# Kernel tuning notes

Hardware: AMD Instinct MI355X
Metric: run time of the kernel (lower is better)

The kernel has to match this reference:

```python
import jax, jax.numpy as jnp
import numpy as np

N_NODES = 100000
N_EDGES = 1600000
IN_DIM, HID_DIM, OUT_DIM = 512, 64, 32


def _gcn_conv(x, row, col, W, b, n):
    # GCNConv: h = x W; out[v] = sum_{(u,v)} norm(u,v) * h[u] + b
    # deg computed on destination (col) with self-loops already included.
    deg = jax.ops.segment_sum(jnp.ones_like(col, dtype=x.dtype), col, num_segments=n)
    dinv = jnp.where(deg > 0, jax.lax.rsqrt(deg), 0.0)
    norm = dinv[row] * dinv[col]                      # [E]
    h = x @ W                                          # [N, out]
    msg = h[row] * norm[:, None]                       # [E, out] gather
    out = jax.ops.segment_sum(msg, col, num_segments=n)  # scatter-add
    return out + b


def setup_inputs() -> dict:
    key = jax.random.key(0)
    k1, k2, k3, k4 = jax.random.split(key, 4)
    x = jax.random.normal(k1, (N_NODES, IN_DIM), dtype=jnp.float32)
    edge_index = jax.random.randint(k2, (2, N_EDGES), 0, N_NODES, dtype=jnp.int64)
    W1 = jax.random.normal(k3, (IN_DIM, HID_DIM), dtype=jnp.float32) / np.sqrt(IN_DIM)
    b1 = jnp.zeros((HID_DIM,), dtype=jnp.float32)
    W2 = jax.random.normal(k4, (HID_DIM, OUT_DIM), dtype=jnp.float32) / np.sqrt(HID_DIM)
    b2 = jnp.zeros((OUT_DIM,), dtype=jnp.float32)
    return {"x": x, "edge_index": edge_index, "W1": W1, "b1": b1, "W2": W2, "b2": b2}


def reference(x, edge_index, W1, b1, W2, b2):
    n = x.shape[0]
    # add self-loops (PyG GCNConv default add_self_loops=True)
    loop = jnp.arange(n, dtype=edge_index.dtype)
    row = jnp.concatenate([edge_index[0], loop])
    col = jnp.concatenate([edge_index[1], loop])
    h = _gcn_conv(x, row, col, W1, b1, n)
    h = jax.nn.relu(h)
    # dropout is identity in eval mode (training=False)
    h = _gcn_conv(h, row, col, W2, b2, n)
    return jax.nn.log_softmax(h, axis=1)
```

## Files before the change

### kernel.cpp

```cpp
#include <hip/hip_runtime.h>


#define IN_DIM 512
#define HID    64
#define OUTD   32

typedef __attribute__((ext_vector_type(8))) short bf16x8;
typedef __attribute__((ext_vector_type(4))) float floatx4;
typedef __attribute__((ext_vector_type(4))) unsigned short ushort4v;
typedef __attribute__((ext_vector_type(8))) unsigned short ushort8v;

__device__ __forceinline__ unsigned short f2bf(float f) {
    unsigned int u = __float_as_uint(f);
    unsigned int r = (u + 0x7fffu + ((u >> 16) & 1u)) >> 16;
    return (unsigned short)r;
}
__device__ __forceinline__ float bf2f(unsigned short h) {
    return __uint_as_float(((unsigned int)h) << 16);
}

__device__ __forceinline__ int eidx(const int* idx32, long long e, int is64) {
    if (is64) { const long long* p = (const long long*)idx32; return (int)p[e]; }
    return idx32[e];
}

__global__ void k_detect(const int* __restrict__ idx, int* __restrict__ flag) {
    if (blockIdx.x == 0 && threadIdx.x == 0) {
        int z = (idx[1] == 0) & (idx[3] == 0) & (idx[5] == 0) & (idx[7] == 0);
        *flag = z;
    }
}

__global__ void k_prepW(const float* __restrict__ W1,
                        unsigned short* __restrict__ W1t_hi,
                        unsigned short* __restrict__ W1t_lo) {
    int t = blockIdx.x * blockDim.x + threadIdx.x;
    if (t < 64 * 512) {
        int n = t >> 9, k = t & 511;
        float v = W1[k * HID + n];
        unsigned short h = f2bf(v);
        W1t_hi[t] = h;
        W1t_lo[t] = f2bf(v - bf2f(h));
    }
}

__global__ void k_zero(int* __restrict__ cnt, int N) {
    int i = blockIdx.x * blockDim.x + threadIdx.x;
    if (i < N) cnt[i] = 0;
}

__global__ void k_count(const int* __restrict__ idx, const int* __restrict__ flag,
                        int* __restrict__ cnt, int E) {
    int e = blockIdx.x * blockDim.x + threadIdx.x;
    if (e >= E) return;
    const int is64 = *flag;
    int c = eidx(idx, (long long)E + e, is64);
    atomicAdd(&cnt[c], 1);
}

__global__ void k_scanA(const int* __restrict__ cnt, int* __restrict__ rowptr,
                        int* __restrict__ part, int N) {
    __shared__ int s[256];
    const int t = threadIdx.x;
    const int i = blockIdx.x * 256 + t;
    int v = (i < N) ? cnt[i] : 0;
    s[t] = v;
    __syncthreads();
#pragma unroll
    for (int off = 1; off < 256; off <<= 1) {
        int x = (t >= off) ? s[t - off] : 0;
        __syncthreads();
        s[t] += x;
        __syncthreads();
    }
    if (i < N) rowptr[i] = s[t] - v;
    if (t == 255) part[blockIdx.x] = s[255];
}

__global__ void k_scanB(const int* __restrict__ part, int* __restrict__ partex, int nb) {
    __shared__ int s[1024];
    const int t = threadIdx.x;
    int v = (t < nb) ? part[t] : 0;
    s[t] = v;
    __syncthreads();
#pragma unroll
    for (int off = 1; off < 1024; off <<= 1) {
        int x = (t >= off) ? s[t - off] : 0;
        __syncthreads();
        s[t] += x;
        __syncthreads();
    }
    partex[t] = s[t] - v;
}

__global__ void k_scanC(int* __restrict__ rowptr, const int* __restrict__ partex,
                        int N, int E) {
    const int i = blockIdx.x * blockDim.x + threadIdx.x;
    if (i < N) rowptr[i] += partex[i >> 8];
    if (i == 0) rowptr[N] = E;
}

__global__ void k_dinv(const int* __restrict__ rowptr, float* __restrict__ dinv, int N) {
    int i = blockIdx.x * blockDim.x + threadIdx.x;
    if (i < N) dinv[i] = rsqrtf((float)(1 + rowptr[i + 1] - rowptr[i]));
}

__global__ void k_place(const int* __restrict__ idx, const int* __restrict__ flag,
                        int* __restrict__ cnt, const int* __restrict__ rowptr,
                        int* __restrict__ src, int E) {
    int e = blockIdx.x * blockDim.x + threadIdx.x;
    if (e >= E) return;
    const int is64 = *flag;
    int r = eidx(idx, e, is64);
    int c = eidx(idx, (long long)E + e, is64);
    int ofs = atomicAdd(&cnt[c], -1) - 1;
    src[rowptr[c] + ofs] = r;
}

__launch_bounds__(256)
__global__ void k_gemm1_mfma(const float* __restrict__ x,
                             const unsigned short* __restrict__ Wt_hi,
                             const unsigned short* __restrict__ Wt_lo,
                             const float* __restrict__ dinv,
                             float* __restrict__ g1, int N) {
    __shared__ unsigned short xs_hi[64 * 72];
    __shared__ unsigned short xs_lo[64 * 72];
    __shared__ unsigned short ws_hi[64 * 72];
    __shared__ unsigned short ws_lo[64 * 72];

    const int t = threadIdx.x;
    const int lane = t & 63;
    const int w = t >> 6;
    const int m = lane & 15;
    const int quad = lane >> 4;
    const int row_base = blockIdx.x * 64;

    const floatx4 zero = {0.0f, 0.0f, 0.0f, 0.0f};
    floatx4 acc[4] = {zero, zero, zero, zero};

    for (int kc = 0; kc < IN_DIM; kc += 64) {
        {
            const int kq = (t & 15) * 4;
#pragma unroll
            for (int p = 0; p < 4; ++p) {
                int rl = (t >> 4) + p * 16;
                int row = row_base + rl;
                if (row > N - 1) row = N - 1;
                float4 v = *(const float4*)(x + (size_t)row * IN_DIM + kc + kq);
                ushort4v hi, lo;
                hi.x = f2bf(v.x); lo.x = f2bf(v.x - bf2f(hi.x));
                hi.y = f2bf(v.y); lo.y = f2bf(v.y - bf2f(hi.y));
                hi.z = f2bf(v.z); lo.z = f2bf(v.z - bf2f(hi.z));
                hi.w = f2bf(v.w); lo.w = f2bf(v.w - bf2f(hi.w));
                *(ushort4v*)&xs_hi[rl * 72 + kq] = hi;
                *(ushort4v*)&xs_lo[rl * 72 + kq] = lo;
            }
        }
        {
            const int nl = t >> 2;
            const int q = (t & 3) * 16;
            const unsigned short* ph = Wt_hi + (size_t)nl * IN_DIM + kc + q;
            const unsigned short* pl = Wt_lo + (size_t)nl * IN_DIM + kc + q;
            *(ushort8v*)&ws_hi[nl * 72 + q]     = *(const ushort8v*)(ph);
            *(ushort8v*)&ws_hi[nl * 72 + q + 8] = *(const ushort8v*)(ph + 8);
            *(ushort8v*)&ws_lo[nl * 72 + q]     = *(const ushort8v*)(pl);
            *(ushort8v*)&ws_lo[nl * 72 + q + 8] = *(const ushort8v*)(pl + 8);
        }
        __syncthreads();
#pragma unroll
        for (int ks = 0; ks < 2; ++ks) {
            const int ko = ks * 32 + quad * 8;
            bf16x8 a_hi = *(const bf16x8*)&xs_hi[(w * 16 + m) * 72 + ko];
            bf16x8 a_lo = *(const bf16x8*)&xs_lo[(w * 16 + m) * 72 + ko];
#pragma unroll
            for (int nt = 0; nt < 4; ++nt) {
                bf16x8 b_hi = *(const bf16x8*)&ws_hi[(nt * 16 + m) * 72 + ko];
                bf16x8 b_lo = *(const bf16x8*)&ws_lo[(nt * 16 + m) * 72 + ko];
                acc[nt] = __builtin_amdgcn_mfma_f32_16x16x32_bf16(a_hi, b_hi, acc[nt], 0, 0, 0);
                acc[nt] = __builtin_amdgcn_mfma_f32_16x16x32_bf16(a_lo, b_hi, acc[nt], 0, 0, 0);
                acc[nt] = __builtin_amdgcn_mfma_f32_16x16x32_bf16(a_hi, b_lo, acc[nt], 0, 0, 0);
            }
        }
        __syncthreads();
    }
#pragma unroll
    for (int r = 0; r < 4; ++r) {
        const int row = row_base + w * 16 + quad * 4 + r;
        if (row < N) {
            const float dv = dinv[row];
#pragma unroll
            for (int nt = 0; nt < 4; ++nt)
                g1[(size_t)row * HID + nt * 16 + m] = acc[nt][r] * dv;
        }
    }
}

__launch_bounds__(256)
__global__ void k_agg1_gemm2(const int* __restrict__ rowptr, const int* __restrict__ src,
                             const float* __restrict__ g1, const float* __restrict__ W2,
                             const float* __restrict__ b1, const float* __restrict__ dinv,
                             float* __restrict__ g2, int N) {
    __shared__ float w2s[HID * OUTD];
    __shared__ float hs[4][HID];

    const int t = threadIdx.x;
    for (int i = t; i < HID * OUTD; i += 256) w2s[i] = W2[i];

    const int w = t >> 6, lane = t & 63;
    const int v = blockIdx.x * 4 + w;
    float dv = 0.0f;
    if (v < N) {
        float acc = g1[(size_t)v * HID + lane];
        int i = rowptr[v];
        const int end = rowptr[v + 1];
        for (; i + 1 < end; i += 2) {
            int r0 = src[i], r1 = src[i + 1];
            acc += g1[(size_t)r0 * HID + lane] + g1[(size_t)r1 * HID + lane];
        }
        if (i < end) acc += g1[(size_t)src[i] * HID + lane];
        dv = dinv[v];
        hs[w][lane] = fmaxf(fmaf(dv, acc, b1[lane]), 0.0f);
    }
    __syncthreads();
    if (v < N) {
        const int j = lane & 31, half = lane >> 5;
        float s = 0.0f;
#pragma unroll
        for (int k = 0; k < 32; ++k) {
            const int kk = half * 32 + k;
            s = fmaf(hs[w][kk], w2s[kk * OUTD + j], s);
        }
        s += __shfl_down(s, 32);
        if (lane < 32) g2[(size_t)v * OUTD + j] = s * dv;
    }
}

__global__ void k_out(const int* __restrict__ rowptr, const int* __restrict__ src,
                      const float* __restrict__ g2, const float* __restrict__ b2,
                      const float* __restrict__ dinv, float* __restrict__ out, int N) {
    const int v = blockIdx.x * 8 + (int)(threadIdx.x >> 5);
    const int j = threadIdx.x & 31;
    if (v >= N) return;
    float acc = g2[(size_t)v * OUTD + j];
    int i = rowptr[v];
    const int end = rowptr[v + 1];
    for (; i + 1 < end; i += 2) {
        int r0 = src[i], r1 = src[i + 1];
        acc += g2[(size_t)r0 * OUTD + j] + g2[(size_t)r1 * OUTD + j];
    }
    if (i < end) acc += g2[(size_t)src[i] * OUTD + j];
    const float z = fmaf(dinv[v], acc, b2[j]);
    float m = z;
#pragma unroll
    for (int d = 16; d; d >>= 1) m = fmaxf(m, __shfl_xor(m, d, 32));
    float s = expf(z - m);
#pragma unroll
    for (int d = 16; d; d >>= 1) s += __shfl_xor(s, d, 32);
    out[(size_t)v * OUTD + j] = z - m - logf(s);
}

extern "C" void kernel_launch(void* const* d_in, const int* in_sizes, int n_in,
                              void* d_out, int out_size, void* d_ws, size_t ws_size,
                              hipStream_t stream) {
    const float* x   = (const float*)d_in[0];
    const int*   idx = (const int*)d_in[1];
    const float* W1  = (const float*)d_in[2];
    const float* b1  = (const float*)d_in[3];
    const float* W2  = (const float*)d_in[4];
    const float* b2  = (const float*)d_in[5];
    float* out = (float*)d_out;

    const int N = in_sizes[0] / IN_DIM;
    const int E = in_sizes[1] / 2;

    unsigned short* W1t_hi = (unsigned short*)d_ws;
    unsigned short* W1t_lo = W1t_hi + 64 * 512;
    int* cnt    = (int*)(W1t_lo + 64 * 512);
    int* rowptr = cnt + N;
    int* part   = rowptr + (N + 4);
    int* partex = part + 1024;
    int* srcA   = partex + 1024;
    int* flag   = srcA + E;
    float* dinv = (float*)(flag + 4);
    float* g1   = dinv + N;
    float* g2   = g1 + (size_t)N * HID;

    const int B = 256;
    const int nb = (N + 255) / 256;

    k_detect<<<1, 64, 0, stream>>>(idx, flag);
    k_prepW<<<(64 * 512 + B - 1) / B, B, 0, stream>>>(W1, W1t_hi, W1t_lo);
    k_zero<<<(N + B - 1) / B, B, 0, stream>>>(cnt, N);
    k_count<<<(E + B - 1) / B, B, 0, stream>>>(idx, flag, cnt, E);
    k_scanA<<<nb, 256, 0, stream>>>(cnt, rowptr, part, N);
    k_scanB<<<1, 1024, 0, stream>>>(part, partex, nb);
    k_scanC<<<nb, 256, 0, stream>>>(rowptr, partex, N, E);
    k_dinv<<<(N + B - 1) / B, B, 0, stream>>>(rowptr, dinv, N);
    k_place<<<(E + B - 1) / B, B, 0, stream>>>(idx, flag, cnt, rowptr, srcA, E);

    k_gemm1_mfma<<<(N + 63) / 64, 256, 0, stream>>>(x, W1t_hi, W1t_lo, dinv, g1, N);
    k_agg1_gemm2<<<(N + 3) / 4, 256, 0, stream>>>(rowptr, srcA, g1, W2, b1, dinv, g2, N);
    k_out<<<(N + 7) / 8, B, 0, stream>>>(rowptr, srcA, g2, b2, dinv, out, N);
}
```

Before: 644.1 us.

## Store intermediates in fp16, merge setup kernels, single-workgroup scan, unroll gathers

Stores the intermediate feature tables g1 and g2 as fp16 instead of fp32, halving the bytes moved by the gather-heavy aggregation kernels. It also merges the flag-detect, W1-prep and zeroing kernels into one launch. The three-stage scan plus dinv kernel is replaced by a single 1024-thread workgroup scan that also writes dinv, and the gather loops are unrolled by four. Precision drops for the intermediates, and the serial per-thread scan chunks (about 98 elements each) may be slower than the parallel scan.

```diff
diff --git a/kernel.cpp b/kernel.cpp
--- a/kernel.cpp
+++ b/kernel.cpp
@@ -1,4 +1,5 @@
 #include <hip/hip_runtime.h>
+#include <hip/hip_fp16.h>
 
 
 #define IN_DIM 512
@@ -24,17 +25,17 @@
     return idx32[e];
 }
 
-__global__ void k_detect(const int* __restrict__ idx, int* __restrict__ flag) {
-    if (blockIdx.x == 0 && threadIdx.x == 0) {
+__global__ void k_init(const float* __restrict__ W1,
+                       unsigned short* __restrict__ W1t_hi,
+                       unsigned short* __restrict__ W1t_lo,
+                       const int* __restrict__ idx, int* __restrict__ flag,
+                       int* __restrict__ cnt, int N) {
+    int t = blockIdx.x * blockDim.x + threadIdx.x;
+    if (t == 0) {
         int z = (idx[1] == 0) & (idx[3] == 0) & (idx[5] == 0) & (idx[7] == 0);
         *flag = z;
     }
-}
-
-__global__ void k_prepW(const float* __restrict__ W1,
-                        unsigned short* __restrict__ W1t_hi,
-                        unsigned short* __restrict__ W1t_lo) {
-    int t = blockIdx.x * blockDim.x + threadIdx.x;
+    if (t < N) cnt[t] = 0;
     if (t < 64 * 512) {
         int n = t >> 9, k = t & 511;
         float v = W1[k * HID + n];
@@ -42,11 +43,6 @@
         W1t_hi[t] = h;
         W1t_lo[t] = f2bf(v - bf2f(h));
     }
-}
-
-__global__ void k_zero(int* __restrict__ cnt, int N) {
-    int i = blockIdx.x * blockDim.x + threadIdx.x;
-    if (i < N) cnt[i] = 0;
 }
 
 __global__ void k_count(const int* __restrict__ idx, const int* __restrict__ flag,
@@ -58,30 +54,16 @@
     atomicAdd(&cnt[c], 1);
 }
 
-__global__ void k_scanA(const int* __restrict__ cnt, int* __restrict__ rowptr,
-                        int* __restrict__ part, int N) {
-    __shared__ int s[256];
-    const int t = threadIdx.x;
-    const int i = blockIdx.x * 256 + t;
-    int v = (i < N) ? cnt[i] : 0;
-    s[t] = v;
-    __syncthreads();
-#pragma unroll
-    for (int off = 1; off < 256; off <<= 1) {
-        int x = (t >= off) ? s[t - off] : 0;
-        __syncthreads();
-        s[t] += x;
-        __syncthreads();
-    }
-    if (i < N) rowptr[i] = s[t] - v;
-    if (t == 255) part[blockIdx.x] = s[255];
-}
-
-__global__ void k_scanB(const int* __restrict__ part, int* __restrict__ partex, int nb) {
+__global__ void k_scan1wg(const int* __restrict__ cnt, int* __restrict__ rowptr,
+                          float* __restrict__ dinv, int N, int E) {
     __shared__ int s[1024];
     const int t = threadIdx.x;
-    int v = (t < nb) ? part[t] : 0;
-    s[t] = v;
+    const int chunk = (N + 1023) / 1024;
+    const int lo = t * chunk;
+    const int hi = (lo + chunk < N) ? lo + chunk : N;
+    int sum = 0;
+    for (int i = lo; i < hi; ++i) sum += cnt[i];
+    s[t] = sum;
     __syncthreads();
 #pragma unroll
     for (int off = 1; off < 1024; off <<= 1) {
@@ -90,19 +72,14 @@
         s[t] += x;
         __syncthreads();
     }
-    partex[t] = s[t] - v;
-}
-
-__global__ void k_scanC(int* __restrict__ rowptr, const int* __restrict__ partex,
-                        int N, int E) {
-    const int i = blockIdx.x * blockDim.x + threadIdx.x;
-    if (i < N) rowptr[i] += partex[i >> 8];
-    if (i == 0) rowptr[N] = E;
-}
-
-__global__ void k_dinv(const int* __restrict__ rowptr, float* __restrict__ dinv, int N) {
-    int i = blockIdx.x * blockDim.x + threadIdx.x;
-    if (i < N) dinv[i] = rsqrtf((float)(1 + rowptr[i + 1] - rowptr[i]));
+    int run = s[t] - sum;
+    for (int i = lo; i < hi; ++i) {
+        int c = cnt[i];
+        rowptr[i] = run;
+        dinv[i] = rsqrtf((float)(1 + c));
+        run += c;
+    }
+    if (t == 0) rowptr[N] = E;
 }
 
 __global__ void k_place(const int* __restrict__ idx, const int* __restrict__ flag,
@@ -122,7 +99,7 @@
                              const unsigned short* __restrict__ Wt_hi,
                              const unsigned short* __restrict__ Wt_lo,
                              const float* __restrict__ dinv,
-                             float* __restrict__ g1, int N) {
+                             __half* __restrict__ g1, int N) {
     __shared__ unsigned short xs_hi[64 * 72];
     __shared__ unsigned short xs_lo[64 * 72];
     __shared__ unsigned short ws_hi[64 * 72];
@@ -190,16 +167,16 @@
             const float dv = dinv[row];
 #pragma unroll
             for (int nt = 0; nt < 4; ++nt)
-                g1[(size_t)row * HID + nt * 16 + m] = acc[nt][r] * dv;
+                g1[(size_t)row * HID + nt * 16 + m] = __float2half(acc[nt][r] * dv);
         }
     }
 }
 
 __launch_bounds__(256)
 __global__ void k_agg1_gemm2(const int* __restrict__ rowptr, const int* __restrict__ src,
-                             const float* __restrict__ g1, const float* __restrict__ W2,
+                             const __half* __restrict__ g1, const float* __restrict__ W2,
                              const float* __restrict__ b1, const float* __restrict__ dinv,
-                             float* __restrict__ g2, int N) {
+                             __half* __restrict__ g2, int N) {
     __shared__ float w2s[HID * OUTD];
     __shared__ float hs[4][HID];
 
@@ -210,14 +187,18 @@
     const int v = blockIdx.x * 4 + w;
     float dv = 0.0f;
     if (v < N) {
-        float acc = g1[(size_t)v * HID + lane];
+        float acc = (float)g1[(size_t)v * HID + lane];
         int i = rowptr[v];
         const int end = rowptr[v + 1];
-        for (; i + 1 < end; i += 2) {
-            int r0 = src[i], r1 = src[i + 1];
-            acc += g1[(size_t)r0 * HID + lane] + g1[(size_t)r1 * HID + lane];
-        }
-        if (i < end) acc += g1[(size_t)src[i] * HID + lane];
+        for (; i + 3 < end; i += 4) {
+            int r0 = src[i], r1 = src[i + 1], r2 = src[i + 2], r3 = src[i + 3];
+            float a0 = (float)g1[(size_t)r0 * HID + lane];
+            float a1 = (float)g1[(size_t)r1 * HID + lane];
+            float a2 = (float)g1[(size_t)r2 * HID + lane];
+            float a3 = (float)g1[(size_t)r3 * HID + lane];
+            acc += (a0 + a1) + (a2 + a3);
+        }
+        for (; i < end; ++i) acc += (float)g1[(size_t)src[i] * HID + lane];
         dv = dinv[v];
         hs[w][lane] = fmaxf(fmaf(dv, acc, b1[lane]), 0.0f);
     }
@@ -231,24 +212,28 @@
             s = fmaf(hs[w][kk], w2s[kk * OUTD + j], s);
         }
         s += __shfl_down(s, 32);
-        if (lane < 32) g2[(size_t)v * OUTD + j] = s * dv;
+        if (lane < 32) g2[(size_t)v * OUTD + j] = __float2half(s * dv);
     }
 }
 
 __global__ void k_out(const int* __restrict__ rowptr, const int* __restrict__ src,
-                      const float* __restrict__ g2, const float* __restrict__ b2,
+                      const __half* __restrict__ g2, const float* __restrict__ b2,
                       const float* __restrict__ dinv, float* __restrict__ out, int N) {
     const int v = blockIdx.x * 8 + (int)(threadIdx.x >> 5);
     const int j = threadIdx.x & 31;
     if (v >= N) return;
-    float acc = g2[(size_t)v * OUTD + j];
+    float acc = (float)g2[(size_t)v * OUTD + j];
     int i = rowptr[v];
     const int end = rowptr[v + 1];
-    for (; i + 1 < end; i += 2) {
-        int r0 = src[i], r1 = src[i + 1];
-        acc += g2[(size_t)r0 * OUTD + j] + g2[(size_t)r1 * OUTD + j];
-    }
-    if (i < end) acc += g2[(size_t)src[i] * OUTD + j];
+    for (; i + 3 < end; i += 4) {
+        int r0 = src[i], r1 = src[i + 1], r2 = src[i + 2], r3 = src[i + 3];
+        float a0 = (float)g2[(size_t)r0 * OUTD + j];
+        float a1 = (float)g2[(size_t)r1 * OUTD + j];
+        float a2 = (float)g2[(size_t)r2 * OUTD + j];
+        float a3 = (float)g2[(size_t)r3 * OUTD + j];
+        acc += (a0 + a1) + (a2 + a3);
+    }
+    for (; i < end; ++i) acc += (float)g2[(size_t)src[i] * OUTD + j];
     const float z = fmaf(dinv[v], acc, b2[j]);
     float m = z;
 #pragma unroll
@@ -277,25 +262,17 @@
     unsigned short* W1t_lo = W1t_hi + 64 * 512;
     int* cnt    = (int*)(W1t_lo + 64 * 512);
     int* rowptr = cnt + N;
-    int* part   = rowptr + (N + 4);
-    int* partex = part + 1024;
-    int* srcA   = partex + 1024;
+    int* srcA   = rowptr + (N + 4);
     int* flag   = srcA + E;
     float* dinv = (float*)(flag + 4);
-    float* g1   = dinv + N;
-    float* g2   = g1 + (size_t)N * HID;
+    __half* g1  = (__half*)(dinv + N);
+    __half* g2  = g1 + (size_t)N * HID;
 
     const int B = 256;
-    const int nb = (N + 255) / 256;
-
-    k_detect<<<1, 64, 0, stream>>>(idx, flag);
-    k_prepW<<<(64 * 512 + B - 1) / B, B, 0, stream>>>(W1, W1t_hi, W1t_lo);
-    k_zero<<<(N + B - 1) / B, B, 0, stream>>>(cnt, N);
+
+    k_init<<<(N + B - 1) / B, B, 0, stream>>>(W1, W1t_hi, W1t_lo, idx, flag, cnt, N);
     k_count<<<(E + B - 1) / B, B, 0, stream>>>(idx, flag, cnt, E);
-    k_scanA<<<nb, 256, 0, stream>>>(cnt, rowptr, part, N);
-    k_scanB<<<1, 1024, 0, stream>>>(part, partex, nb);
-    k_scanC<<<nb, 256, 0, stream>>>(rowptr, partex, N, E);
-    k_dinv<<<(N + B - 1) / B, B, 0, stream>>>(rowptr, dinv, N);
+    k_scan1wg<<<1, 1024, 0, stream>>>(cnt, rowptr, dinv, N, E);
     k_place<<<(E + B - 1) / B, B, 0, stream>>>(idx, flag, cnt, rowptr, srcA, E);
 
     k_gemm1_mfma<<<(N + 63) / 64, 256, 0, stream>>>(x, W1t_hi, W1t_lo, dinv, g1, N);
```

Result: slower. 798.3 us (+23.9%).
